# Performance work log

Measured on AMD Instinct MI355X. Metric: run time of the kernel, lower is better.

Reference implementation:

```python
import jax, jax.numpy as jnp
import numpy as np

HEADS = 8
DIM_HEAD = 64
ROT_DIM = DIM_HEAD // 2  # RotaryEmbedding(dim=head_dim//2) rotates first 32 dims of each head
THETA = 10000.0


def _rope_cos_sin(T, dtype):
    # rotary_embedding_torch: freqs = 1/theta**(arange(0,dim,2)/dim), len dim//2,
    # angles repeated interleaved across pairs -> (T, ROT_DIM)
    inv = 1.0 / (THETA ** (jnp.arange(0, ROT_DIM, 2, dtype=jnp.float32) / ROT_DIM))
    ang = jnp.arange(T, dtype=jnp.float32)[:, None] * inv[None, :]      # (T, ROT_DIM/2)
    ang = jnp.repeat(ang, 2, axis=-1)                                   # (T, ROT_DIM) interleaved
    return jnp.cos(ang).astype(dtype), jnp.sin(ang).astype(dtype)


def _rotate_half(x):
    # pairs (x1, x2) -> (-x2, x1), interleaved layout '... (d 2)'
    x = x.reshape(x.shape[:-1] + (-1, 2))
    x = jnp.stack([-x[..., 1], x[..., 0]], axis=-1)
    return x.reshape(x.shape[:-2] + (-1,))


def _apply_rope(x, cos, sin):
    # x: (N, h, T, dh); rotate first ROT_DIM dims, pass through the rest
    xr, xp = x[..., :ROT_DIM], x[..., ROT_DIM:]
    xr = xr * cos[None, None, :, :] + _rotate_half(xr) * sin[None, None, :, :]
    return jnp.concatenate([xr, xp], axis=-1)


def setup_inputs() -> dict:
    key = jax.random.key(0)
    k1, k2, k3 = jax.random.split(key, 3)
    B, T, H, W, D = 2, 32, 32, 32, 512
    inner = HEADS * DIM_HEAD
    x = jax.random.normal(k1, (B, T, H, W, D), dtype=jnp.float32)
    w_qkv = jax.random.normal(k2, (D, 3 * inner), dtype=jnp.float32) * (D ** -0.5)
    w_out = jax.random.normal(k3, (inner, D), dtype=jnp.float32) * (inner ** -0.5)
    b_out = jnp.zeros((D,), dtype=jnp.float32)
    return {"x": x, "w_qkv": w_qkv, "w_out": w_out, "b_out": b_out}


def reference(x, w_qkv, w_out, b_out):
    B, T, H, W, D = x.shape
    qkv = jnp.einsum('bthwd,de->bthwe', x, w_qkv)               # (B,T,H,W,3*inner)
    q, k, v = jnp.split(qkv, 3, axis=-1)

    def to_axial(t):  # (B,T,H,W,inner) -> (B*H*W, heads, T, dh)
        t = t.reshape(B, T, H, W, HEADS, DIM_HEAD)
        t = jnp.transpose(t, (0, 2, 3, 4, 1, 5))
        return t.reshape(B * H * W, HEADS, T, DIM_HEAD)

    q, k, v = to_axial(q), to_axial(k), to_axial(v)
    cos, sin = _rope_cos_sin(T, x.dtype)
    q = _apply_rope(q, cos, sin)
    k = _apply_rope(k, cos, sin)

    scale = DIM_HEAD ** -0.5
    scores = jnp.einsum('nhqd,nhkd->nhqk', q, k) * scale        # (N,h,T,T)
    causal = jnp.tril(jnp.ones((T, T), dtype=bool))
    scores = jnp.where(causal[None, None, :, :], scores, jnp.finfo(scores.dtype).min)
    attn = jax.nn.softmax(scores, axis=-1)
    out = jnp.einsum('nhqk,nhkd->nhqd', attn, v)                # (N,h,T,dh)

    out = out.reshape(B, H, W, HEADS, T, DIM_HEAD)
    out = jnp.transpose(out, (0, 4, 1, 2, 3, 5)).reshape(B, T, H, W, HEADS * DIM_HEAD)
    return jnp.einsum('bthwe,ed->bthwd', out, w_out) + b_out
```

## Files before the change

### kernel.cpp

```cpp
#include <hip/hip_runtime.h>
#include <hip/hip_bf16.h>
#include <math.h>

#define HEADS  8
#define TT     32
#define DMODEL 512
#define HWSZ   1024
#define TSTRIDE (HWSZ*DMODEL)

#define NQKV (3*DMODEL*DMODEL)
#define NOUT (DMODEL*DMODEL)
#define NTAB 512

typedef __attribute__((ext_vector_type(8))) short bf16x8;
typedef __attribute__((ext_vector_type(4))) float f32x4;
typedef __attribute__((ext_vector_type(4))) short s16x4;

__device__ __forceinline__ unsigned short f2bf(float f) {
    unsigned int u = __builtin_bit_cast(unsigned int, f);
    u += 0x7FFFu + ((u >> 16) & 1u);
    return (unsigned short)(u >> 16);
}

__global__ __launch_bounds__(256)
void taa_prep(const float* __restrict__ wqkv, const float* __restrict__ wout,
              unsigned short* __restrict__ ws) {
    long i = (long)blockIdx.x * 256 + threadIdx.x;
    unsigned short* wqf = ws;
    unsigned short* wof = ws + NQKV;
    float* cs = (float*)(wof + NOUT);
    float* sn = cs + NTAB;
    if (i < NQKV) {
        int i8 = (int)(i & 7), lane = (int)((i >> 3) & 63), blk = (int)(i >> 9);
        int k05 = blk & 15, t = blk >> 4;
        int n = t * 16 + (lane & 15);
        int k = k05 * 32 + (lane >> 4) * 8 + i8;
        wqf[i] = f2bf(wqkv[(long)k * 1536 + n]);
    } else if (i < NQKV + NOUT) {
        long j = i - NQKV;
        int i8 = (int)(j & 7), lane = (int)((j >> 3) & 63), blk = (int)(j >> 9);
        int k05 = blk & 15, t = blk >> 4;
        int col = t * 16 + (lane & 15);
        int k = k05 * 32 + (lane >> 4) * 8 + i8;
        wof[j] = f2bf(wout[(long)k * 512 + col]);
    } else if (i < NQKV + NOUT + NTAB) {
        int j = (int)(i - NQKV - NOUT);
        int t = j >> 4, f = j & 15;
        float inv = powf(10000.f, -(float)(2 * f) / 32.f);
        float sv, cv;
        sincosf((float)t * inv, &sv, &cv);
        cs[j] = cv; sn[j] = sv;
    }
}

#define X_OFF  0
#define Q_OFF  65536
#define K_OFF  73728
#define V_OFF  81920
#define P_OFF  98304
#define PV_OFF 106496
#define S_OFF  114688
#define CS_OFF 123136
#define SN_OFF 125184
#define LDS_SZ 127232

#define XS(g, r, cB) (X_OFF + ((g) << 15) + ((r) << 10) + ((cB) ^ (((r) & 7) << 4)))
#define RS(base, r, cB) ((base) + ((r) << 7) + ((cB) ^ (((r) & 7) << 4)))

#define MFMA(a, b, c) __builtin_amdgcn_mfma_f32_16x16x32_bf16((a), (b), (c), 0, 0, 0)

__global__ __launch_bounds__(512, 2)
void taa_main(const float* __restrict__ x,
              const unsigned short* __restrict__ ws,
              const float* __restrict__ b_out,
              float* __restrict__ out) {
    extern __shared__ __align__(16) unsigned char smem[];

    const unsigned short* wqf = ws;
    const unsigned short* wof = ws + NQKV;
    const float* cs_gl = (const float*)(wof + NOUT);
    const float* sn_gl = cs_gl + NTAB;

    const int tid  = threadIdx.x;
    const int lane = tid & 63;
    const int wv   = tid >> 6;
    const int quad = lane >> 4;
    const int lid  = lane & 15;

    const int n0 = blockIdx.x * 2;
    const long long base0 = ((long long)(n0 >> 10) * (TT * HWSZ) + (n0 & 1023)) * DMODEL;
    const int n1 = n0 + 1;
    const long long base1 = ((long long)(n1 >> 10) * (TT * HWSZ) + (n1 & 1023)) * DMODEL;

    float* cs_l = (float*)(smem + CS_OFF);
    float* sn_l = (float*)(smem + SN_OFF);
    for (int i = tid; i < NTAB; i += 512) { cs_l[i] = cs_gl[i]; sn_l[i] = sn_gl[i]; }

    for (int idx = tid; idx < 4096; idx += 512) {
        int g  = idx >> 11;
        int r  = (idx >> 6) & 31;
        int c8 = idx & 63;
        long long bg = g ? base1 : base0;
        const float4* src = (const float4*)(x + bg + (long long)r * TSTRIDE + c8 * 8);
        float4 f0 = src[0], f1 = src[1];
        s16x4 lo, hi;
        lo[0] = (short)f2bf(f0.x); lo[1] = (short)f2bf(f0.y);
        lo[2] = (short)f2bf(f0.z); lo[3] = (short)f2bf(f0.w);
        hi[0] = (short)f2bf(f1.x); hi[1] = (short)f2bf(f1.y);
        hi[2] = (short)f2bf(f1.z); hi[3] = (short)f2bf(f1.w);
        int a = XS(g, r, c8 * 16);
        *(s16x4*)(smem + a)     = lo;
        *(s16x4*)(smem + a + 8) = hi;
    }

    f32x4 oacc[4][2][2];
    #pragma unroll
    for (int j = 0; j < 4; ++j)
        #pragma unroll
        for (int g = 0; g < 2; ++g)
            #pragma unroll
            for (int mt = 0; mt < 2; ++mt) oacc[j][g][mt] = (f32x4){0.f, 0.f, 0.f, 0.f};

    __syncthreads();

    for (int h = 0; h < HEADS; ++h) {
        for (int rnd = 0; rnd < 2; ++rnd) {
            if (rnd == 1 && wv >= 4) break;
            int ct  = (rnd == 0) ? wv : 8 + wv;
            int m   = ct >> 2;
            int t16 = ct & 3;
            int T   = m * 32 + h * 4 + t16;
            const unsigned short* wp = wqf + ((long)T * 16) * 512 + lane * 8;
            f32x4 acc[2][2];
            #pragma unroll
            for (int g = 0; g < 2; ++g)
                #pragma unroll
                for (int mt = 0; mt < 2; ++mt) acc[g][mt] = (f32x4){0.f, 0.f, 0.f, 0.f};
            #pragma unroll 4
            for (int k05 = 0; k05 < 16; ++k05) {
                bf16x8 bw = *(const bf16x8*)(wp + (long)k05 * 512);
                #pragma unroll
                for (int g = 0; g < 2; ++g)
                    #pragma unroll
                    for (int mt = 0; mt < 2; ++mt) {
                        bf16x8 a = *(const bf16x8*)(smem + XS(g, lid + 16 * mt, k05 * 64 + quad * 16));
                        acc[g][mt] = MFMA(a, bw, acc[g][mt]);
                    }
            }
            if (m < 2) {
                int dstb = (m == 0) ? Q_OFF : K_OFF;
                if (t16 < 2) {
                    #pragma unroll
                    for (int g = 0; g < 2; ++g)
                        #pragma unroll
                        for (int mt = 0; mt < 2; ++mt)
                            #pragma unroll
                            for (int r = 0; r < 4; ++r) {
                                float v = acc[g][mt][r];
                                float p = __shfl_xor(v, 1, 64);
                                int trow = mt * 16 + quad * 4 + r;
                                int colh = t16 * 16 + lid;
                                int jj = colh >> 1;
                                float cv = cs_l[trow * 16 + jj];
                                float sv = sn_l[trow * 16 + jj];
                                float res = (colh & 1) ? (v * cv + p * sv) : (v * cv - p * sv);
                                *(unsigned short*)(smem + RS(dstb + g * 4096, trow, colh * 2)) = f2bf(res);
                            }
                } else {
                    #pragma unroll
                    for (int g = 0; g < 2; ++g)
                        #pragma unroll
                        for (int mt = 0; mt < 2; ++mt)
                            #pragma unroll
                            for (int r = 0; r < 4; ++r) {
                                int trow = mt * 16 + quad * 4 + r;
                                *(unsigned short*)(smem + RS(dstb + g * 4096, trow, (t16 * 16 + lid) * 2)) = f2bf(acc[g][mt][r]);
                            }
                }
            } else {
                #pragma unroll
                for (int g = 0; g < 2; ++g)
                    #pragma unroll
                    for (int mt = 0; mt < 2; ++mt) {
                        int d  = t16 * 16 + lid;
                        int t0 = mt * 16 + quad * 4;
                        s16x4 pk;
                        pk[0] = (short)f2bf(acc[g][mt][0]); pk[1] = (short)f2bf(acc[g][mt][1]);
                        pk[2] = (short)f2bf(acc[g][mt][2]); pk[3] = (short)f2bf(acc[g][mt][3]);
                        *(s16x4*)(smem + RS(V_OFF + g * 8192, d, t0 * 2)) = pk;
                    }
            }
        }
        __syncthreads();

        {
            int g = wv >> 2, mt = (wv >> 1) & 1, nt = wv & 1;
            f32x4 acc = {0.f, 0.f, 0.f, 0.f};
            #pragma unroll
            for (int d05 = 0; d05 < 2; ++d05) {
                bf16x8 a  = *(const bf16x8*)(smem + RS(Q_OFF + g * 4096, lid + 16 * mt, d05 * 64 + quad * 16));
                bf16x8 bk = *(const bf16x8*)(smem + RS(K_OFF + g * 4096, lid + 16 * nt, d05 * 64 + quad * 16));
                acc = MFMA(a, bk, acc);
            }
            float* sg = (float*)(smem + S_OFF + g * 4224);
            #pragma unroll
            for (int r = 0; r < 4; ++r)
                sg[(mt * 16 + quad * 4 + r) * 33 + nt * 16 + lid] = acc[r] * 0.125f;
        }
        __syncthreads();

        {
            int row = tid >> 3;
            int g = row >> 5, r = row & 31;
            int sub = tid & 7;
            const float* sg = (const float*)(smem + S_OFF + g * 4224);
            float vals[4];
            float mx = -1e30f;
            #pragma unroll
            for (int jj = 0; jj < 4; ++jj) {
                int cc = sub * 4 + jj;
                float v = (cc <= r) ? sg[r * 33 + cc] : -1e30f;
                vals[jj] = v;
                mx = fmaxf(mx, v);
            }
            mx = fmaxf(mx, __shfl_xor(mx, 1, 64));
            mx = fmaxf(mx, __shfl_xor(mx, 2, 64));
            mx = fmaxf(mx, __shfl_xor(mx, 4, 64));
            float sum = 0.f;
            #pragma unroll
            for (int jj = 0; jj < 4; ++jj) {
                int cc = sub * 4 + jj;
                float e = (cc <= r) ? __expf(vals[jj] - mx) : 0.f;
                vals[jj] = e;
                sum += e;
            }
            sum += __shfl_xor(sum, 1, 64);
            sum += __shfl_xor(sum, 2, 64);
            sum += __shfl_xor(sum, 4, 64);
            float rs = 1.f / sum;
            s16x4 pk;
            #pragma unroll
            for (int jj = 0; jj < 4; ++jj) pk[jj] = (short)f2bf(vals[jj] * rs);
            *(s16x4*)(smem + RS(P_OFF + g * 4096, r, sub * 8)) = pk;
        }
        __syncthreads();

        {
            int g = wv >> 2, mt = (wv >> 1) & 1, ntp = (wv & 1) * 2;
            bf16x8 a = *(const bf16x8*)(smem + RS(P_OFF + g * 4096, lid + 16 * mt, quad * 16));
            #pragma unroll
            for (int j = 0; j < 2; ++j) {
                int nt = ntp + j;
                bf16x8 bv = *(const bf16x8*)(smem + RS(V_OFF + g * 8192, nt * 16 + lid, quad * 16));
                f32x4 acc = MFMA(a, bv, ((f32x4){0.f, 0.f, 0.f, 0.f}));
                #pragma unroll
                for (int r = 0; r < 4; ++r) {
                    int t = mt * 16 + quad * 4 + r;
                    int d = nt * 16 + lid;
                    *(unsigned short*)(smem + RS(PV_OFF + g * 4096, t, d * 2)) = f2bf(acc[r]);
                }
            }
        }
        __syncthreads();

        {
            #pragma unroll
            for (int k05h = 0; k05h < 2; ++k05h) {
                int kb = h * 2 + k05h;
                bf16x8 a[2][2];
                #pragma unroll
                for (int g = 0; g < 2; ++g)
                    #pragma unroll
                    for (int mt = 0; mt < 2; ++mt)
                        a[g][mt] = *(const bf16x8*)(smem + RS(PV_OFF + g * 4096, lid + 16 * mt, k05h * 64 + quad * 16));
                #pragma unroll
                for (int j = 0; j < 4; ++j) {
                    int ct = wv + 8 * j;
                    bf16x8 bw = *(const bf16x8*)(wof + ((long)(ct * 16 + kb)) * 512 + lane * 8);
                    #pragma unroll
                    for (int g = 0; g < 2; ++g)
                        #pragma unroll
                        for (int mt = 0; mt < 2; ++mt)
                            oacc[j][g][mt] = MFMA(a[g][mt], bw, oacc[j][g][mt]);
                }
            }
        }
        __syncthreads();
    }

    #pragma unroll
    for (int j = 0; j < 4; ++j) {
        int col = (wv + 8 * j) * 16 + lid;
        float bias = b_out[col];
        #pragma unroll
        for (int g = 0; g < 2; ++g) {
            long long bg = g ? base1 : base0;
            #pragma unroll
            for (int mt = 0; mt < 2; ++mt)
                #pragma unroll
                for (int r = 0; r < 4; ++r) {
                    int t = mt * 16 + quad * 4 + r;
                    out[bg + (long long)t * TSTRIDE + col] = oacc[j][g][mt][r] + bias;
                }
        }
    }
}

extern "C" void kernel_launch(void* const* d_in, const int* in_sizes, int n_in,
                              void* d_out, int out_size, void* d_ws, size_t ws_size,
                              hipStream_t stream) {
    const float* x     = (const float*)d_in[0];
    const float* w_qkv = (const float*)d_in[1];
    const float* w_out = (const float*)d_in[2];
    const float* b_out = (const float*)d_in[3];
    float* out = (float*)d_out;
    (void)in_sizes; (void)n_in; (void)out_size; (void)ws_size;

    unsigned short* ws = (unsigned short*)d_ws;

    taa_prep<<<dim3(4098), dim3(256), 0, stream>>>(w_qkv, w_out, ws);
    taa_main<<<dim3(1024), dim3(512), LDS_SZ, stream>>>(x, ws, b_out, out);
}
```

Measured before the change: 272.8 us.

## Process head pairs per iteration and fuse QK, softmax, PV into one 32x32 MFMA stage

Each loop iteration now processes two heads, so the QKV projection uses all 8 waves across three full rounds instead of leaving half the waves idle in the second round. The separate QK^T, softmax and PV stages, with their LDS score and probability buffers, are merged into one per-wave stage using 32x32x16 MFMAs, with softmax done in registers. This drops two barriers and the LDS round-trips per head. LDS use grows past the two-blocks-per-CU budget, so launch bounds drop to one block per CU and occupancy falls. The trailing barrier was also removed, which risks a race between the next iteration's Q/K/V writes and the output-projection reads of PV.

```diff
diff --git a/kernel.cpp b/kernel.cpp
--- a/kernel.cpp
+++ b/kernel.cpp
@@ -12,9 +12,10 @@
 #define NOUT (DMODEL*DMODEL)
 #define NTAB 512
 
-typedef __attribute__((ext_vector_type(8))) short bf16x8;
-typedef __attribute__((ext_vector_type(4))) float f32x4;
-typedef __attribute__((ext_vector_type(4))) short s16x4;
+typedef __attribute__((ext_vector_type(8)))  short bf16x8;
+typedef __attribute__((ext_vector_type(4)))  float f32x4;
+typedef __attribute__((ext_vector_type(16))) float f32x16;
+typedef __attribute__((ext_vector_type(4)))  short s16x4;
 
 __device__ __forceinline__ unsigned short f2bf(float f) {
     unsigned int u = __builtin_bit_cast(unsigned int, f);
@@ -55,21 +56,21 @@
 
 #define X_OFF  0
 #define Q_OFF  65536
-#define K_OFF  73728
-#define V_OFF  81920
-#define P_OFF  98304
-#define PV_OFF 106496
-#define S_OFF  114688
-#define CS_OFF 123136
-#define SN_OFF 125184
-#define LDS_SZ 127232
+#define K_OFF  81920
+#define V_OFF  98304
+#define PV_OFF 114688
+#define CS_OFF 131072
+#define SN_OFF 133120
+#define LDS_SZ 135168
 
 #define XS(g, r, cB) (X_OFF + ((g) << 15) + ((r) << 10) + ((cB) ^ (((r) & 7) << 4)))
 #define RS(base, r, cB) ((base) + ((r) << 7) + ((cB) ^ (((r) & 7) << 4)))
-
-#define MFMA(a, b, c) __builtin_amdgcn_mfma_f32_16x16x32_bf16((a), (b), (c), 0, 0, 0)
-
-__global__ __launch_bounds__(512, 2)
+#define VS(base, d, cB) ((base) + ((d) << 6) + ((cB) ^ (((d) & 7) << 3)))
+
+#define MFMA16(a, b, c) __builtin_amdgcn_mfma_f32_16x16x32_bf16((a), (b), (c), 0, 0, 0)
+#define MFMA32(a, b, c) __builtin_amdgcn_mfma_f32_32x32x16_bf16((a), (b), (c), 0, 0, 0)
+
+__global__ __launch_bounds__(512, 1)
 void taa_main(const float* __restrict__ x,
               const unsigned short* __restrict__ ws,
               const float* __restrict__ b_out,
@@ -123,13 +124,15 @@
 
     __syncthreads();
 
-    for (int h = 0; h < HEADS; ++h) {
-        for (int rnd = 0; rnd < 2; ++rnd) {
-            if (rnd == 1 && wv >= 4) break;
-            int ct  = (rnd == 0) ? wv : 8 + wv;
-            int m   = ct >> 2;
+    for (int it = 0; it < 4; ++it) {
+        const int hpair = it * 2;
+
+        for (int rnd = 0; rnd < 3; ++rnd) {
+            int ct  = rnd * 8 + wv;
+            int m   = ct >> 3;
+            int hh  = (ct >> 2) & 1;
             int t16 = ct & 3;
-            int T   = m * 32 + h * 4 + t16;
+            int T   = m * 32 + (hpair + hh) * 4 + t16;
             const unsigned short* wp = wqf + ((long)T * 16) * 512 + lane * 8;
             f32x4 acc[2][2];
             #pragma unroll
@@ -144,11 +147,11 @@
                     #pragma unroll
                     for (int mt = 0; mt < 2; ++mt) {
                         bf16x8 a = *(const bf16x8*)(smem + XS(g, lid + 16 * mt, k05 * 64 + quad * 16));
-                        acc[g][mt] = MFMA(a, bw, acc[g][mt]);
+                        acc[g][mt] = MFMA16(a, bw, acc[g][mt]);
                     }
             }
             if (m < 2) {
-                int dstb = (m == 0) ? Q_OFF : K_OFF;
+                int dstb = ((m == 0) ? Q_OFF : K_OFF) + hh * 4096;
                 if (t16 < 2) {
                     #pragma unroll
                     for (int g = 0; g < 2; ++g)
@@ -164,7 +167,7 @@
                                 float cv = cs_l[trow * 16 + jj];
                                 float sv = sn_l[trow * 16 + jj];
                                 float res = (colh & 1) ? (v * cv + p * sv) : (v * cv - p * sv);
-                                *(unsigned short*)(smem + RS(dstb + g * 4096, trow, colh * 2)) = f2bf(res);
+                                *(unsigned short*)(smem + RS(dstb + g * 8192, trow, colh * 2)) = f2bf(res);
                             }
                 } else {
                     #pragma unroll
@@ -174,7 +177,7 @@
                             #pragma unroll
                             for (int r = 0; r < 4; ++r) {
                                 int trow = mt * 16 + quad * 4 + r;
-                                *(unsigned short*)(smem + RS(dstb + g * 4096, trow, (t16 * 16 + lid) * 2)) = f2bf(acc[g][mt][r]);
+                                *(unsigned short*)(smem + RS(dstb + g * 8192, trow, (t16 * 16 + lid) * 2)) = f2bf(acc[g][mt][r]);
                             }
                 }
             } else {
@@ -187,92 +190,93 @@
                         s16x4 pk;
                         pk[0] = (short)f2bf(acc[g][mt][0]); pk[1] = (short)f2bf(acc[g][mt][1]);
                         pk[2] = (short)f2bf(acc[g][mt][2]); pk[3] = (short)f2bf(acc[g][mt][3]);
-                        *(s16x4*)(smem + RS(V_OFF + g * 8192, d, t0 * 2)) = pk;
+                        *(s16x4*)(smem + VS(V_OFF + (g * 2 + hh) * 4096, d, t0 * 2)) = pk;
                     }
             }
         }
         __syncthreads();
 
         {
-            int g = wv >> 2, mt = (wv >> 1) & 1, nt = wv & 1;
-            f32x4 acc = {0.f, 0.f, 0.f, 0.f};
-            #pragma unroll
-            for (int d05 = 0; d05 < 2; ++d05) {
-                bf16x8 a  = *(const bf16x8*)(smem + RS(Q_OFF + g * 4096, lid + 16 * mt, d05 * 64 + quad * 16));
-                bf16x8 bk = *(const bf16x8*)(smem + RS(K_OFF + g * 4096, lid + 16 * nt, d05 * 64 + quad * 16));
-                acc = MFMA(a, bk, acc);
-            }
-            float* sg = (float*)(smem + S_OFF + g * 4224);
-            #pragma unroll
-            for (int r = 0; r < 4; ++r)
-                sg[(mt * 16 + quad * 4 + r) * 33 + nt * 16 + lid] = acc[r] * 0.125f;
+            int g  = wv >> 2;
+            int hh = (wv >> 1) & 1;
+            int dt = wv & 1;
+            int qr  = Q_OFF  + (g * 2 + hh) * 4096;
+            int kr  = K_OFF  + (g * 2 + hh) * 4096;
+            int vr  = V_OFF  + (g * 2 + hh) * 4096;
+            int pvr = PV_OFF + (g * 2 + hh) * 4096;
+            int tq = lane & 31;
+            int hf = lane >> 5;
+
+            f32x16 sc = {0.f,0.f,0.f,0.f,0.f,0.f,0.f,0.f,0.f,0.f,0.f,0.f,0.f,0.f,0.f,0.f};
+            #pragma unroll
+            for (int j = 0; j < 4; ++j) {
+                bf16x8 aK = *(const bf16x8*)(smem + RS(kr, tq, j * 32 + hf * 16));
+                bf16x8 bQ = *(const bf16x8*)(smem + RS(qr, tq, j * 32 + hf * 16));
+                sc = MFMA32(aK, bQ, sc);
+            }
+            float pe[16];
+            float mx = -1e30f;
+            #pragma unroll
+            for (int r = 0; r < 16; ++r) {
+                int tk = (r & 3) + 8 * (r >> 2) + 4 * hf;
+                float v = (tk <= tq) ? sc[r] * 0.125f : -1e30f;
+                pe[r] = v;
+                mx = fmaxf(mx, v);
+            }
+            mx = fmaxf(mx, __shfl_xor(mx, 32, 64));
+            float sum = 0.f;
+            #pragma unroll
+            for (int r = 0; r < 16; ++r) {
+                float e = __expf(pe[r] - mx);
+                pe[r] = e;
+                sum += e;
+            }
+            sum += __shfl_xor(sum, 32, 64);
+            float inv = 1.f / sum;
+            bf16x8 pa0, pa1;
+            #pragma unroll
+            for (int i = 0; i < 8; ++i) {
+                pa0[i] = (short)f2bf(pe[i] * inv);
+                pa1[i] = (short)f2bf(pe[8 + i] * inv);
+            }
+            int d = dt * 32 + tq;
+            f32x16 o = {0.f,0.f,0.f,0.f,0.f,0.f,0.f,0.f,0.f,0.f,0.f,0.f,0.f,0.f,0.f,0.f};
+            {
+                s16x4 lo = *(const s16x4*)(smem + VS(vr, d, 8 * hf));
+                s16x4 hi = *(const s16x4*)(smem + VS(vr, d, 16 + 8 * hf));
+                bf16x8 bv;
+                bv[0] = lo[0]; bv[1] = lo[1]; bv[2] = lo[2]; bv[3] = lo[3];
+                bv[4] = hi[0]; bv[5] = hi[1]; bv[6] = hi[2]; bv[7] = hi[3];
+                o = MFMA32(pa0, bv, o);
+            }
+            {
+                s16x4 lo = *(const s16x4*)(smem + VS(vr, d, 32 + 8 * hf));
+                s16x4 hi = *(const s16x4*)(smem + VS(vr, d, 48 + 8 * hf));
+                bf16x8 bv;
+                bv[0] = lo[0]; bv[1] = lo[1]; bv[2] = lo[2]; bv[3] = lo[3];
+                bv[4] = hi[0]; bv[5] = hi[1]; bv[6] = hi[2]; bv[7] = hi[3];
+                o = MFMA32(pa1, bv, o);
+            }
+            #pragma unroll
+            for (int r = 0; r < 16; ++r) {
+                int t = (r & 3) + 8 * (r >> 2) + 4 * hf;
+                *(unsigned short*)(smem + RS(pvr, t, 2 * d)) = f2bf(o[r]);
+            }
         }
         __syncthreads();
 
         {
-            int row = tid >> 3;
-            int g = row >> 5, r = row & 31;
-            int sub = tid & 7;
-            const float* sg = (const float*)(smem + S_OFF + g * 4224);
-            float vals[4];
-            float mx = -1e30f;
-            #pragma unroll
-            for (int jj = 0; jj < 4; ++jj) {
-                int cc = sub * 4 + jj;
-                float v = (cc <= r) ? sg[r * 33 + cc] : -1e30f;
-                vals[jj] = v;
-                mx = fmaxf(mx, v);
-            }
-            mx = fmaxf(mx, __shfl_xor(mx, 1, 64));
-            mx = fmaxf(mx, __shfl_xor(mx, 2, 64));
-            mx = fmaxf(mx, __shfl_xor(mx, 4, 64));
-            float sum = 0.f;
-            #pragma unroll
-            for (int jj = 0; jj < 4; ++jj) {
-                int cc = sub * 4 + jj;
-                float e = (cc <= r) ? __expf(vals[jj] - mx) : 0.f;
-                vals[jj] = e;
-                sum += e;
-            }
-            sum += __shfl_xor(sum, 1, 64);
-            sum += __shfl_xor(sum, 2, 64);
-            sum += __shfl_xor(sum, 4, 64);
-            float rs = 1.f / sum;
-            s16x4 pk;
-            #pragma unroll
-            for (int jj = 0; jj < 4; ++jj) pk[jj] = (short)f2bf(vals[jj] * rs);
-            *(s16x4*)(smem + RS(P_OFF + g * 4096, r, sub * 8)) = pk;
-        }
-        __syncthreads();
-
-        {
-            int g = wv >> 2, mt = (wv >> 1) & 1, ntp = (wv & 1) * 2;
-            bf16x8 a = *(const bf16x8*)(smem + RS(P_OFF + g * 4096, lid + 16 * mt, quad * 16));
-            #pragma unroll
-            for (int j = 0; j < 2; ++j) {
-                int nt = ntp + j;
-                bf16x8 bv = *(const bf16x8*)(smem + RS(V_OFF + g * 8192, nt * 16 + lid, quad * 16));
-                f32x4 acc = MFMA(a, bv, ((f32x4){0.f, 0.f, 0.f, 0.f}));
-                #pragma unroll
-                for (int r = 0; r < 4; ++r) {
-                    int t = mt * 16 + quad * 4 + r;
-                    int d = nt * 16 + lid;
-                    *(unsigned short*)(smem + RS(PV_OFF + g * 4096, t, d * 2)) = f2bf(acc[r]);
-                }
-            }
-        }
-        __syncthreads();
-
-        {
-            #pragma unroll
-            for (int k05h = 0; k05h < 2; ++k05h) {
-                int kb = h * 2 + k05h;
+            #pragma unroll
+            for (int k05h = 0; k05h < 4; ++k05h) {
+                int hh   = k05h >> 1;
+                int dblk = k05h & 1;
+                int kb   = (hpair + hh) * 2 + dblk;
                 bf16x8 a[2][2];
                 #pragma unroll
                 for (int g = 0; g < 2; ++g)
                     #pragma unroll
                     for (int mt = 0; mt < 2; ++mt)
-                        a[g][mt] = *(const bf16x8*)(smem + RS(PV_OFF + g * 4096, lid + 16 * mt, k05h * 64 + quad * 16));
+                        a[g][mt] = *(const bf16x8*)(smem + RS(PV_OFF + (g * 2 + hh) * 4096, lid + 16 * mt, dblk * 64 + quad * 16));
                 #pragma unroll
                 for (int j = 0; j < 4; ++j) {
                     int ct = wv + 8 * j;
@@ -281,11 +285,10 @@
                     for (int g = 0; g < 2; ++g)
                         #pragma unroll
                         for (int mt = 0; mt < 2; ++mt)
-                            oacc[j][g][mt] = MFMA(a[g][mt], bw, oacc[j][g][mt]);
+                            oacc[j][g][mt] = MFMA16(a[g][mt], bw, oacc[j][g][mt]);
                 }
             }
         }
-        __syncthreads();
     }
 
     #pragma unroll
```

Measured after the change: 239.4 us. 1.14x faster.
